# Kernel optimization log

Measured on AMD Instinct MI355X. Metric: run time of the kernel, lower is better.

Reference implementation:

```python
import jax, jax.numpy as jnp
import numpy as np

B, S, U, H = 4, 2048, 1024, 16
DH = U // H  # head dim = 64
EPS = 1e-8


def setup_inputs() -> dict:
    key = jax.random.key(0)
    ks = jax.random.split(key, 7)
    scale = 1.0 / np.sqrt(U)
    return {
        "queries": jax.random.normal(ks[0], (B, S, U), jnp.float32),
        "keys": jax.random.normal(ks[1], (B, S, U), jnp.float32),
        "values": jax.random.normal(ks[2], (B, S, U), jnp.float32),
        "Wq": jax.random.normal(ks[3], (U, U), jnp.float32) * scale,
        "bq": jnp.zeros((U,), jnp.float32),
        "Wk": jax.random.normal(ks[4], (U, U), jnp.float32) * scale,
        "bk": jnp.zeros((U,), jnp.float32),
        "Wv": jax.random.normal(ks[5], (U, U), jnp.float32) * scale,
        "bv": jnp.zeros((U,), jnp.float32),
        "Wr": jax.random.normal(ks[6], (U, U), jnp.float32) * scale,
        "br": jnp.zeros((U,), jnp.float32),
        "gamma": jnp.ones((U,), jnp.float32),
        "beta": jnp.zeros((U,), jnp.float32),
    }


def reference(queries, keys, values, Wq, bq, Wk, bk, Wv, bv, Wr, br, gamma, beta):
    relu = jax.nn.relu
    Q = relu(queries @ Wq + bq)           # [B,S,U]
    K = relu(keys @ Wk + bk)
    V = relu(values @ Wv + bv)
    V_res = relu(values @ Wr + br)        # residual branch

    # split heads: tf.split(axis=2) + concat(axis=0) == per-head attention
    Qh = Q.reshape(B, S, H, DH)
    Kh = K.reshape(B, S, H, DH)
    Vh = V.reshape(B, S, H, DH)

    scores = jnp.einsum("bshd,bthd->bhst", Qh, Kh) / jnp.sqrt(jnp.float32(DH))
    w = jax.nn.softmax(scores, axis=-1)   # dropout keep_prob=1 -> identity
    out = jnp.einsum("bhst,bthd->bshd", w, Vh).reshape(B, S, U)

    out = relu(out + V_res)

    # manual LayerNorm (eps inside sqrt)
    mean = jnp.mean(out, axis=-1, keepdims=True)
    var = jnp.mean(jnp.square(out - mean), axis=-1, keepdims=True)
    normalized = (out - mean) / jnp.sqrt(var + EPS)
    return gamma * normalized + beta
```

## Files before the change

kernel.cpp:

```cpp
#include <hip/hip_runtime.h>

constexpr int B = 4, S = 2048, U = 1024, H = 16, DH = 64;
constexpr int MTOT = B * S;
constexpr int NT = S / 64;

using bf16   = __bf16;
using f32x4  = __attribute__((ext_vector_type(4))) float;
using f32x16 = __attribute__((ext_vector_type(16))) float;
using bf16x8 = __attribute__((ext_vector_type(8))) bf16;
using bf16x4 = __attribute__((ext_vector_type(4))) bf16;
using u32x4  = __attribute__((ext_vector_type(4))) unsigned int;

__device__ __forceinline__ void gload16(const bf16* g, bf16* l) {
  __builtin_amdgcn_global_load_lds(
      (const __attribute__((address_space(1))) unsigned int*)g,
      (__attribute__((address_space(3))) unsigned int*)l, 16, 0, 0);
}

__device__ __forceinline__ float fexp2(float x) {
#if __has_builtin(__builtin_amdgcn_exp2f)
  return __builtin_amdgcn_exp2f(x);
#else
  return __expf(x * 0.6931471805599453f);
#endif
}

__device__ __forceinline__ f32x16 mfma32(bf16x8 a, bf16x8 b, f32x16 c) {
  return __builtin_amdgcn_mfma_f32_32x32x16_bf16(a, b, c, 0, 0, 0);
}

__device__ __forceinline__ unsigned packbf(float a, float b) {
  union { bf16 h; unsigned short s; } ua, ub;
  ua.h = (bf16)a; ub.h = (bf16)b;
  return ((unsigned)ub.s << 16) | (unsigned)ua.s;
}

__device__ __forceinline__ size_t kpack_off(int M_, int col) {
  const int b = M_ >> 11, s = M_ & 2047;
  const int h = col >> 6, d = col & 63;
  const int bh = b * 16 + h;
  const int t = s >> 6, r64 = s & 63;
  const int tt = r64 >> 5, l31 = r64 & 31;
  const int ks = d >> 4, hi = (d >> 3) & 1, j = d & 7;
  const int ln = l31 + (hi << 5);
  return ((size_t)(bh * 32 + t) << 12) + (tt << 11) + (ks << 9) + (ln << 3) + j;
}

__device__ __forceinline__ size_t vpack_off(int M_, int col) {
  const int b = M_ >> 11, s = M_ & 2047;
  const int h = col >> 6, d = col & 63;
  const int bh = b * 16 + h;
  const int j = s & 7, hi = (s >> 3) & 1, ks = (s >> 4) & 3, t = s >> 6;
  const int dt = d >> 5, l31 = d & 31;
  const int ln = l31 + (hi << 5);
  return ((size_t)(bh * 32 + t) << 12) + (dt << 11) + (ks << 9) + (ln << 3) + j;
}

__global__ __launch_bounds__(256) void prep_kernel(
    const float* __restrict__ xq, const float* __restrict__ xk, const float* __restrict__ xv,
    bf16* __restrict__ oq, bf16* __restrict__ ok, bf16* __restrict__ ov,
    const float* __restrict__ w0, const float* __restrict__ w1,
    const float* __restrict__ w2, const float* __restrict__ w3,
    bf16* __restrict__ t0, bf16* __restrict__ t1,
    bf16* __restrict__ t2, bf16* __restrict__ t3) {
  __shared__ float tile[32][33];
  const int bid = blockIdx.x;
  const int t = threadIdx.x;
  if (bid < 12288) {
    const int z = bid >> 12, idx = bid & 4095;
    const float* x = z == 0 ? xq : z == 1 ? xk : xv;
    bf16* o       = z == 0 ? oq : z == 1 ? ok : ov;
    const size_t i = ((size_t)idx * 256 + t) * 8;
    const float4 v0 = *reinterpret_cast<const float4*>(x + i);
    const float4 v1 = *reinterpret_cast<const float4*>(x + i + 4);
    bf16x8 r;
    r[0] = (bf16)v0.x; r[1] = (bf16)v0.y; r[2] = (bf16)v0.z; r[3] = (bf16)v0.w;
    r[4] = (bf16)v1.x; r[5] = (bf16)v1.y; r[6] = (bf16)v1.z; r[7] = (bf16)v1.w;
    *reinterpret_cast<bf16x8*>(o + i) = r;
  } else {
    const int wb = bid - 12288;
    const int z = wb >> 10, ti = wb & 1023;
    const float* W = z == 0 ? w0 : z == 1 ? w1 : z == 2 ? w2 : w3;
    bf16* Wt       = z == 0 ? t0 : z == 1 ? t1 : z == 2 ? t2 : t3;
    const int k0 = (ti & 31) * 32, n0 = (ti >> 5) * 32;
    const int tx = t & 31, ty = t >> 5;
    for (int i = ty; i < 32; i += 8) tile[i][tx] = W[(size_t)(k0 + i) * U + n0 + tx];
    __syncthreads();
    for (int i = ty; i < 32; i += 8) Wt[(size_t)(n0 + i) * U + k0 + tx] = (bf16)tile[tx][i];
  }
}

__global__ __launch_bounds__(256) void gemm4_kernel(
    const bf16* __restrict__ Qc, const bf16* __restrict__ Kc, const bf16* __restrict__ Vc,
    const bf16* __restrict__ wqt, const bf16* __restrict__ wkt,
    const bf16* __restrict__ wvt, const bf16* __restrict__ wrt,
    const float* __restrict__ bq, const float* __restrict__ bk,
    const float* __restrict__ bv, const float* __restrict__ br,
    bf16* __restrict__ oq, bf16* __restrict__ okp,
    bf16* __restrict__ ovp, bf16* __restrict__ orr) {
  const int bid = blockIdx.x;
  const int wg = (bid & 7) * 256 + (bid >> 3);
  const int z = wg >> 9, rem = wg & 511;
  const int bm = (rem >> 3) * 128, bn = (rem & 7) * 128;

  const bf16* A     = z == 0 ? Qc : z == 1 ? Kc : Vc;
  const bf16* Wt    = z == 0 ? wqt : z == 1 ? wkt : z == 2 ? wvt : wrt;
  const float* bias = z == 0 ? bq : z == 1 ? bk : z == 2 ? bv : br;

  const int t = threadIdx.x, lane = t & 63, wid = t >> 6;
  const int wr = wid >> 1, wc = wid & 1;
  const int lm = lane & 15, hi = lane >> 4;

  __shared__ __align__(16) bf16 As[128][64];
  __shared__ __align__(16) bf16 Bs[128][64];

  f32x4 acc[4][4];
#pragma unroll
  for (int i = 0; i < 4; ++i)
#pragma unroll
    for (int j = 0; j < 4; ++j) acc[i][j] = f32x4{0.f, 0.f, 0.f, 0.f};

  const int lr = lane >> 3;
  const int scol = ((lane & 7) ^ lr) * 8;
  const bf16* ga = A  + (size_t)(bm + wid * 32 + lr) * U + scol;
  const bf16* gb = Wt + (size_t)(bn + wid * 32 + lr) * U + scol;

  for (int k0 = 0; k0 < U; k0 += 64) {
    __syncthreads();
#pragma unroll
    for (int p = 0; p < 4; ++p) {
      gload16(ga + (size_t)(p * 8) * U + k0, &As[wid * 32 + p * 8][0]);
      gload16(gb + (size_t)(p * 8) * U + k0, &Bs[wid * 32 + p * 8][0]);
    }
    __syncthreads();

#pragma unroll
    for (int ksub = 0; ksub < 2; ++ksub) {
      const int so = (((ksub * 4 + hi) ^ (lm & 7)) * 16);
      bf16x8 a[4], bb[4];
#pragma unroll
      for (int mi = 0; mi < 4; ++mi)
        a[mi] = *reinterpret_cast<const bf16x8*>(
            reinterpret_cast<const char*>(&As[wr * 64 + mi * 16 + lm][0]) + so);
#pragma unroll
      for (int ni = 0; ni < 4; ++ni)
        bb[ni] = *reinterpret_cast<const bf16x8*>(
            reinterpret_cast<const char*>(&Bs[wc * 64 + ni * 16 + lm][0]) + so);
#pragma unroll
      for (int mi = 0; mi < 4; ++mi)
#pragma unroll
        for (int ni = 0; ni < 4; ++ni)
          acc[mi][ni] = __builtin_amdgcn_mfma_f32_16x16x32_bf16(a[mi], bb[ni], acc[mi][ni], 0, 0, 0);
    }
  }

  const int mb = bm + wr * 64 + hi * 4;
  const int nb = bn + wc * 64 + lm;
  if (z == 1) {
#pragma unroll
    for (int ni = 0; ni < 4; ++ni) {
      const float bv_ = bias[nb + ni * 16];
#pragma unroll
      for (int mi = 0; mi < 4; ++mi)
#pragma unroll
        for (int r = 0; r < 4; ++r) {
          const float vv = fmaxf(acc[mi][ni][r] + bv_, 0.f);
          okp[kpack_off(mb + mi * 16 + r, nb + ni * 16)] = (bf16)vv;
        }
    }
  } else if (z == 2) {
#pragma unroll
    for (int ni = 0; ni < 4; ++ni) {
      const float bv_ = bias[nb + ni * 16];
#pragma unroll
      for (int mi = 0; mi < 4; ++mi)
#pragma unroll
        for (int r = 0; r < 4; ++r) {
          const float vv = fmaxf(acc[mi][ni][r] + bv_, 0.f);
          ovp[vpack_off(mb + mi * 16 + r, nb + ni * 16)] = (bf16)vv;
        }
    }
  } else {
    bf16* out = z == 0 ? oq : orr;
#pragma unroll
    for (int ni = 0; ni < 4; ++ni) {
      const float bv_ = bias[nb + ni * 16];
#pragma unroll
      for (int mi = 0; mi < 4; ++mi)
#pragma unroll
        for (int r = 0; r < 4; ++r) {
          const float vv = fmaxf(acc[mi][ni][r] + bv_, 0.f);
          out[(size_t)(mb + mi * 16 + r) * U + nb + ni * 16] = (bf16)vv;
        }
    }
  }
}

__global__ __launch_bounds__(256) void attn_kernel(
    const bf16* __restrict__ Q, const bf16* __restrict__ Kp,
    const bf16* __restrict__ Vp, bf16* __restrict__ att) {
  const int bid = blockIdx.x;
  const int swz = (bid & 7) * 128 + (bid >> 3);
  const int bh = swz >> 4, qx = swz & 15;
  const int b = bh >> 4, h = bh & 15;
  const int tid = threadIdx.x;
  const int w = tid >> 6, lane = tid & 63;
  const int l31 = lane & 31, hi8 = lane >> 5;
  const int q0 = qx * 128 + w * 32;

  const float qscale = 0.18033688011111606f;

  const bf16* qbase = Q + ((size_t)b * S + q0 + l31) * U + h * DH + hi8 * 8;
  bf16x8 qf[4];
#pragma unroll
  for (int ks = 0; ks < 4; ++ks) {
    bf16x8 v = *reinterpret_cast<const bf16x8*>(qbase + ks * 16);
#pragma unroll
    for (int j = 0; j < 8; ++j) v[j] = (bf16)((float)v[j] * qscale);
    qf[ks] = v;
  }

  bf16x8 onesf;
#pragma unroll
  for (int j = 0; j < 8; ++j) onesf[j] = (bf16)1.f;

  f32x16 o0 = (f32x16)0.f, o1 = (f32x16)0.f, osum = (f32x16)0.f;

  const bf16* kl = Kp + (size_t)bh * 32 * 4096 + lane * 8;
  const bf16* vl = Vp + (size_t)bh * 32 * 4096 + lane * 8;

  bf16x8 kf[2][4];
#pragma unroll
  for (int tt = 0; tt < 2; ++tt)
#pragma unroll
    for (int ks = 0; ks < 4; ++ks)
      kf[tt][ks] = *reinterpret_cast<const bf16x8*>(kl + (tt * 4 + ks) * 512);

  for (int t = 0; t < NT; ++t) {
    bf16x8 vf[2][4];
#pragma unroll
    for (int dt = 0; dt < 2; ++dt)
#pragma unroll
      for (int ks = 0; ks < 4; ++ks)
        vf[dt][ks] = *reinterpret_cast<const bf16x8*>(vl + (size_t)t * 4096 + (dt * 4 + ks) * 512);

    f32x16 s0 = (f32x16)0.f, s1 = (f32x16)0.f;
    __builtin_amdgcn_s_setprio(1);
#pragma unroll
    for (int ks = 0; ks < 4; ++ks) {
      s0 = mfma32(kf[0][ks], qf[ks], s0);
      s1 = mfma32(kf[1][ks], qf[ks], s1);
    }
    __builtin_amdgcn_s_setprio(0);

    if (t + 1 < NT) {
#pragma unroll
      for (int tt = 0; tt < 2; ++tt)
#pragma unroll
        for (int ks = 0; ks < 4; ++ks)
          kf[tt][ks] = *reinterpret_cast<const bf16x8*>(
              kl + (size_t)(t + 1) * 4096 + (tt * 4 + ks) * 512);
    }

    unsigned wpk[16];
#pragma unroll
    for (int i = 0; i < 8; ++i) {
      wpk[i]     = packbf(fexp2(s0[2 * i]), fexp2(s0[2 * i + 1]));
      wpk[8 + i] = packbf(fexp2(s1[2 * i]), fexp2(s1[2 * i + 1]));
    }

    u32x4 fw[4];
#pragma unroll
    for (int fi = 0; fi < 4; ++fi) {
      unsigned a0 = wpk[fi * 4 + 0], b0 = wpk[fi * 4 + 2];
      unsigned a1 = wpk[fi * 4 + 1], b1 = wpk[fi * 4 + 3];
      asm("v_permlane32_swap_b32 %0, %1" : "+v"(a0), "+v"(b0));
      asm("v_permlane32_swap_b32 %0, %1" : "+v"(a1), "+v"(b1));
      fw[fi] = u32x4{a0, a1, b0, b1};
    }

    __builtin_amdgcn_s_setprio(1);
#pragma unroll
    for (int ks = 0; ks < 4; ++ks) {
      const bf16x8 pf = __builtin_bit_cast(bf16x8, fw[ks]);
      o0   = mfma32(pf, vf[0][ks], o0);
      o1   = mfma32(pf, vf[1][ks], o1);
      osum = mfma32(pf, onesf, osum);
    }
    __builtin_amdgcn_s_setprio(0);
  }

  bf16* obase = att + ((size_t)b * S + q0) * U + h * DH + l31;
#pragma unroll
  for (int r = 0; r < 16; ++r) {
    const int row = (r & 3) + 8 * (r >> 2) + 4 * hi8;
    const float lr = 1.f / osum[r];
    obase[(size_t)row * U]      = (bf16)(o0[r] * lr);
    obase[(size_t)row * U + 32] = (bf16)(o1[r] * lr);
  }
}

__global__ __launch_bounds__(256) void ln_kernel(
    const bf16* __restrict__ att, const bf16* __restrict__ vres,
    const float* __restrict__ gamma, const float* __restrict__ beta,
    float* __restrict__ out) {
  const int row = blockIdx.x;
  const int t = threadIdx.x;
  const bf16* ar = att + (size_t)row * U;
  const bf16* vr = vres + (size_t)row * U;
  const bf16x4 av = *reinterpret_cast<const bf16x4*>(ar + t * 4);
  const bf16x4 vv = *reinterpret_cast<const bf16x4*>(vr + t * 4);
  float x[4];
  float sum = 0.f, sq = 0.f;
#pragma unroll
  for (int i = 0; i < 4; ++i) {
    x[i] = fmaxf((float)av[i] + (float)vv[i], 0.f);
    sum += x[i];
    sq += x[i] * x[i];
  }
#pragma unroll
  for (int mm = 1; mm < 64; mm <<= 1) {
    sum += __shfl_xor(sum, mm);
    sq  += __shfl_xor(sq, mm);
  }
  __shared__ float s1[4], s2[4];
  if ((t & 63) == 0) { s1[t >> 6] = sum; s2[t >> 6] = sq; }
  __syncthreads();
  sum = s1[0] + s1[1] + s1[2] + s1[3];
  sq  = s2[0] + s2[1] + s2[2] + s2[3];
  const float mean = sum * (1.f / U);
  float var = sq * (1.f / U) - mean * mean;
  var = fmaxf(var, 0.f);
  const float inv = rsqrtf(var + 1e-8f);
#pragma unroll
  for (int i = 0; i < 4; ++i) {
    const int c = t * 4 + i;
    out[(size_t)row * U + c] = gamma[c] * ((x[i] - mean) * inv) + beta[c];
  }
}

extern "C" void kernel_launch(void* const* d_in, const int* in_sizes, int n_in,
                              void* d_out, int out_size, void* d_ws, size_t ws_size,
                              hipStream_t stream) {
  const float* queries = (const float*)d_in[0];
  const float* keys    = (const float*)d_in[1];
  const float* values  = (const float*)d_in[2];
  const float* Wq = (const float*)d_in[3];
  const float* bq = (const float*)d_in[4];
  const float* Wk = (const float*)d_in[5];
  const float* bk = (const float*)d_in[6];
  const float* Wv = (const float*)d_in[7];
  const float* bv = (const float*)d_in[8];
  const float* Wr = (const float*)d_in[9];
  const float* br = (const float*)d_in[10];
  const float* gamma = (const float*)d_in[11];
  const float* beta  = (const float*)d_in[12];
  float* out = (float*)d_out;

  char* ws = (char*)d_ws;
  const size_t MB = 1024 * 1024;
  bf16* wqt  = (bf16*)(ws + 0 * MB);
  bf16* wkt  = (bf16*)(ws + 2 * MB);
  bf16* wvt  = (bf16*)(ws + 4 * MB);
  bf16* wrt  = (bf16*)(ws + 6 * MB);
  bf16* Qcvt = (bf16*)(ws + 8 * MB);
  bf16* Kcvt = (bf16*)(ws + 24 * MB);
  bf16* Vcvt = (bf16*)(ws + 40 * MB);
  bf16* Qb   = (bf16*)(ws + 56 * MB);
  bf16* Kp   = (bf16*)(ws + 72 * MB);
  bf16* Vp   = (bf16*)(ws + 88 * MB);
  bf16* attb = Qcvt;
  bf16* Rb   = Kcvt;

  prep_kernel<<<dim3(16384), 256, 0, stream>>>(
      queries, keys, values, Qcvt, Kcvt, Vcvt,
      Wq, Wk, Wv, Wr, wqt, wkt, wvt, wrt);
  gemm4_kernel<<<dim3(2048), 256, 0, stream>>>(
      Qcvt, Kcvt, Vcvt, wqt, wkt, wvt, wrt, bq, bk, bv, br, Qb, Kp, Vp, Rb);
  attn_kernel<<<dim3(1024), 256, 0, stream>>>(Qb, Kp, Vp, attb);
  ln_kernel<<<dim3(MTOT), 256, 0, stream>>>(attb, Rb, gamma, beta, out);
}
```

Baseline: 230.9 us.

## Stage K/V tiles through double-buffered LDS shared across waves

The attention kernel previously had each of the four waves load the same K and V tiles straight from global memory into registers. It now cooperatively copies each K/V tile into a double-buffered LDS region using global_load_lds, prefetching the next tile while the current one is computed. A barrier at the end of each iteration synchronises the buffers. The aim is to cut redundant global/L2 traffic by four, at the cost of LDS reads, per-tile barriers, 32 KB of LDS per block, and a launch-bounds occupancy hint.

```diff
diff --git a/kernel.cpp b/kernel.cpp
--- a/kernel.cpp
+++ b/kernel.cpp
@@ -196,7 +196,7 @@
   }
 }
 
-__global__ __launch_bounds__(256) void attn_kernel(
+__global__ __launch_bounds__(256, 2) void attn_kernel(
     const bf16* __restrict__ Q, const bf16* __restrict__ Kp,
     const bf16* __restrict__ Vp, bf16* __restrict__ att) {
   const int bid = blockIdx.x;
@@ -208,6 +208,8 @@
   const int l31 = lane & 31, hi8 = lane >> 5;
   const int q0 = qx * 128 + w * 32;
 
+  __shared__ __align__(16) bf16 kv[2][8192];
+
   const float qscale = 0.18033688011111606f;
 
   const bf16* qbase = Q + ((size_t)b * S + q0 + l31) * U + h * DH + hi8 * 8;
@@ -226,23 +228,32 @@
 
   f32x16 o0 = (f32x16)0.f, o1 = (f32x16)0.f, osum = (f32x16)0.f;
 
-  const bf16* kl = Kp + (size_t)bh * 32 * 4096 + lane * 8;
-  const bf16* vl = Vp + (size_t)bh * 32 * 4096 + lane * 8;
-
-  bf16x8 kf[2][4];
-#pragma unroll
-  for (int tt = 0; tt < 2; ++tt)
-#pragma unroll
-    for (int ks = 0; ks < 4; ++ks)
-      kf[tt][ks] = *reinterpret_cast<const bf16x8*>(kl + (tt * 4 + ks) * 512);
+  const bf16* kpb = Kp + (size_t)bh * 32 * 4096;
+  const bf16* vpb = Vp + (size_t)bh * 32 * 4096;
+
+  auto stagekv = [&](int buf, int t) {
+    const size_t toff = (size_t)t * 4096;
+    gload16(kpb + toff + tid * 8,        &kv[buf][tid * 8]);
+    gload16(kpb + toff + 2048 + tid * 8, &kv[buf][2048 + tid * 8]);
+    gload16(vpb + toff + tid * 8,        &kv[buf][4096 + tid * 8]);
+    gload16(vpb + toff + 2048 + tid * 8, &kv[buf][6144 + tid * 8]);
+  };
+
+  stagekv(0, 0);
+  asm volatile("s_waitcnt vmcnt(0)" ::: "memory");
+  __builtin_amdgcn_s_barrier();
+  __builtin_amdgcn_sched_barrier(0);
 
   for (int t = 0; t < NT; ++t) {
-    bf16x8 vf[2][4];
-#pragma unroll
-    for (int dt = 0; dt < 2; ++dt)
+    const int cur = t & 1;
+    if (t + 1 < NT) stagekv(cur ^ 1, t + 1);
+
+    bf16x8 kf[2][4];
+#pragma unroll
+    for (int tt = 0; tt < 2; ++tt)
 #pragma unroll
       for (int ks = 0; ks < 4; ++ks)
-        vf[dt][ks] = *reinterpret_cast<const bf16x8*>(vl + (size_t)t * 4096 + (dt * 4 + ks) * 512);
+        kf[tt][ks] = *reinterpret_cast<const bf16x8*>(&kv[cur][(tt * 4 + ks) * 512 + lane * 8]);
 
     f32x16 s0 = (f32x16)0.f, s1 = (f32x16)0.f;
     __builtin_amdgcn_s_setprio(1);
@@ -253,14 +264,12 @@
     }
     __builtin_amdgcn_s_setprio(0);
 
-    if (t + 1 < NT) {
-#pragma unroll
-      for (int tt = 0; tt < 2; ++tt)
-#pragma unroll
-        for (int ks = 0; ks < 4; ++ks)
-          kf[tt][ks] = *reinterpret_cast<const bf16x8*>(
-              kl + (size_t)(t + 1) * 4096 + (tt * 4 + ks) * 512);
-    }
+    bf16x8 vf[2][4];
+#pragma unroll
+    for (int dt = 0; dt < 2; ++dt)
+#pragma unroll
+      for (int ks = 0; ks < 4; ++ks)
+        vf[dt][ks] = *reinterpret_cast<const bf16x8*>(&kv[cur][4096 + (dt * 4 + ks) * 512 + lane * 8]);
 
     unsigned wpk[16];
 #pragma unroll
@@ -288,6 +297,12 @@
       osum = mfma32(pf, onesf, osum);
     }
     __builtin_amdgcn_s_setprio(0);
+
+    if (t + 1 < NT) {
+      asm volatile("s_waitcnt vmcnt(0)" ::: "memory");
+      __builtin_amdgcn_s_barrier();
+      __builtin_amdgcn_sched_barrier(0);
+    }
   }
 
   bf16* obase = att + ((size_t)b * S + q0) * U + h * DH + l31;
```

Result: faster. 206.4 us (-10.6%).
